# Optimization experiments

Hardware: AMD Instinct MI355X
Metric: run time of the kernel (lower is better)

## Reference

```python
import jax, jax.numpy as jnp
import numpy as np

T, B, I, H = 2048, 256, 64, 128


def setup_inputs() -> dict:
    key = jax.random.key(0)
    ks = jax.random.split(key, 12)
    s_i = 1.0 / np.sqrt(I)
    s_h = 1.0 / np.sqrt(H)
    return {
        "x": jax.random.normal(ks[0], (T, B, I), dtype=jnp.float32),
        # input->hidden kernels (with bias), flax GRUCell naming ir/iz/in
        "Wir": jax.random.normal(ks[1], (I, H), dtype=jnp.float32) * s_i,
        "Wiz": jax.random.normal(ks[2], (I, H), dtype=jnp.float32) * s_i,
        "Win": jax.random.normal(ks[3], (I, H), dtype=jnp.float32) * s_i,
        "bir": jnp.zeros((H,), dtype=jnp.float32),
        "biz": jnp.zeros((H,), dtype=jnp.float32),
        "bin": jnp.zeros((H,), dtype=jnp.float32),
        # hidden->hidden kernels: hr/hz no bias, hn has bias (flax GRUCell)
        "Whr": jax.random.normal(ks[4], (H, H), dtype=jnp.float32) * s_h,
        "Whz": jax.random.normal(ks[5], (H, H), dtype=jnp.float32) * s_h,
        "Whn": jax.random.normal(ks[6], (H, H), dtype=jnp.float32) * s_h,
        "bhn": jnp.zeros((H,), dtype=jnp.float32),
        # classifier Linear(H, 1)
        "Wc": jax.random.normal(ks[7], (H, 1), dtype=jnp.float32) * s_h,
        "bc": jnp.zeros((1,), dtype=jnp.float32),
    }


def reference(x, Wir, Wiz, Win, bir, biz, bin, Whr, Whz, Whn, bhn, Wc, bc):
    # GRU scan over time (time-major), flax GRUCell math:
    # r = sig(x Wir + bir + h Whr); z = sig(x Wiz + biz + h Whz)
    def step(h, xt):
        r = jax.nn.sigmoid(xt @ Wir + bir + h @ Whr)
        z = jax.nn.sigmoid(xt @ Wiz + biz + h @ Whz)
        n = jnp.tanh(xt @ Win + bin + r * (h @ Whn + bhn))
        h_new = (1.0 - z) * n + z * h
        return h_new, h_new

    h0 = jnp.zeros((x.shape[1], Whr.shape[0]), dtype=x.dtype)
    _, hs = jax.lax.scan(step, h0, x)  # hs: [T, B, H]
    return jax.nn.sigmoid(hs @ Wc + bc)  # [T, B, 1]
```

## Files before the change

kernel.cpp:

```cpp
#include <hip/hip_runtime.h>

#define TT 2048
#define BB 256
#define II 64
#define HH 128
#define CHP 16
#define NCH (TT / CHP)
#define GXS 532

#define LOG2E  1.4426950408889634f
#define LOG2E2 2.8853900817779268f

typedef __fp16 f16;
typedef __fp16 h2  __attribute__((ext_vector_type(2)));
typedef __fp16 v8h __attribute__((ext_vector_type(8)));
typedef float  v4f __attribute__((ext_vector_type(4)));
typedef int    v4i __attribute__((ext_vector_type(4)));

union HI { int i; h2 h; };
__device__ __forceinline__ h2  i2h(int v) { HI u; u.i = v; return u.h; }
__device__ __forceinline__ int h2i(h2 v)  { HI u; u.h = v; return u.i; }

__device__ __forceinline__ float fexp2(float x) {
  float r; asm("v_exp_f32 %0, %1" : "=v"(r) : "v"(x)); return r;
}
__device__ __forceinline__ float fsig(float x) {
  return __builtin_amdgcn_rcpf(1.0f + __expf(-x));
}

__device__ __forceinline__ void bar_lgkm() {
  asm volatile("s_waitcnt lgkmcnt(0)\n\ts_barrier" ::: "memory");
}

template <int CLS>
__global__ __launch_bounds__(512, 1) void gru_mfma(
    const float* __restrict__ x,
    const float* __restrict__ Wir, const float* __restrict__ Wiz, const float* __restrict__ Win,
    const float* __restrict__ bir, const float* __restrict__ biz, const float* __restrict__ bin_,
    const float* __restrict__ Whr, const float* __restrict__ Whz, const float* __restrict__ Whn,
    const float* __restrict__ bhn, const float* __restrict__ Wc,  const float* __restrict__ bc,
    f16* __restrict__ hh, float* __restrict__ out)
{
  const int t = threadIdx.x, b = blockIdx.x;
  const int w = t >> 6;
  const int l = t & 63;
  const int q = l >> 4;
  const int r = l & 15;
  const int nc = 16 * w + r;

  __shared__ __attribute__((aligned(16))) signed char hq8[2][HH];
  __shared__ __attribute__((aligned(16))) f16   xch[2][CHP][72];
  __shared__ __attribute__((aligned(16))) float gxb[2][CHP][GXS];
  __shared__ float cpart[2][128];

  v4i bqr[2], bqz[2], bqn[2];
  float invR, invZ, invN;
  {
    float mr = 1e-20f, mz = 1e-20f, mn = 1e-20f;
    for (int f = 0; f < 2; ++f)
      for (int j = 0; j < 16; ++j) {
        const int k = 64 * f + 16 * q + j;
        mr = fmaxf(mr, fabsf(Whr[k * HH + nc]));
        mz = fmaxf(mz, fabsf(Whz[k * HH + nc]));
        mn = fmaxf(mn, fabsf(Whn[k * HH + nc]));
      }
    mr = fmaxf(mr, __shfl_xor(mr, 16, 64)); mr = fmaxf(mr, __shfl_xor(mr, 32, 64));
    mz = fmaxf(mz, __shfl_xor(mz, 16, 64)); mz = fmaxf(mz, __shfl_xor(mz, 32, 64));
    mn = fmaxf(mn, __shfl_xor(mn, 16, 64)); mn = fmaxf(mn, __shfl_xor(mn, 32, 64));
    const float sr = 127.f / mr, sz = 127.f / mz, sn = 127.f / mn;
    invR = LOG2E  * mr / 16129.f;
    invZ = LOG2E  * mz / 16129.f;
    invN = LOG2E2 * mn / 16129.f;
    for (int f = 0; f < 2; ++f) {
      union { signed char c[16]; v4i v; } ur, uz, un;
      for (int j = 0; j < 16; ++j) {
        const int k = 64 * f + 16 * q + j;
        ur.c[j] = (signed char)(int)rintf(Whr[k * HH + nc] * sr);
        uz.c[j] = (signed char)(int)rintf(Whz[k * HH + nc] * sz);
        un.c[j] = (signed char)(int)rintf(Whn[k * HH + nc] * sn);
      }
      bqr[f] = ur.v; bqz[f] = uz.v; bqn[f] = un.v;
    }
  }

  v8h wir[2], wiz[2], win2[2];
  for (int kt = 0; kt < 2; ++kt) {
    v8h vr, vz, vn;
    for (int j = 0; j < 8; ++j) {
      const int kg = 32 * kt + 8 * q + j;
      vr[j] = (f16)(LOG2E  * Wir[kg * HH + nc]);
      vz[j] = (f16)(LOG2E  * Wiz[kg * HH + nc]);
      vn[j] = (f16)(LOG2E2 * Win[kg * HH + nc]);
    }
    wir[kt] = vr; wiz[kt] = vz; win2[kt] = vn;
  }

  const float birc = LOG2E * bir[nc],  bizc = LOG2E * biz[nc];
  const float binc = LOG2E2 * bin_[nc], bhnc = LOG2E2 * bhn[nc];
  float wc = 0.f, bc0 = 0.f;
  if (CLS == 1) { wc = Wc[nc]; bc0 = bc[0]; }

  auto precomp_full = [&](int pn, v8h ax0, v8h ax1) {
    v4f cr = {birc, birc, birc, birc};
    v4f cz = {bizc, bizc, bizc, bizc};
    v4f cn = {binc, binc, binc, binc};
    cr = __builtin_amdgcn_mfma_f32_16x16x32_f16(ax0, wir[0],  cr, 0, 0, 0);
    cz = __builtin_amdgcn_mfma_f32_16x16x32_f16(ax0, wiz[0],  cz, 0, 0, 0);
    cn = __builtin_amdgcn_mfma_f32_16x16x32_f16(ax0, win2[0], cn, 0, 0, 0);
    cr = __builtin_amdgcn_mfma_f32_16x16x32_f16(ax1, wir[1],  cr, 0, 0, 0);
    cz = __builtin_amdgcn_mfma_f32_16x16x32_f16(ax1, wiz[1],  cz, 0, 0, 0);
    cn = __builtin_amdgcn_mfma_f32_16x16x32_f16(ax1, win2[1], cn, 0, 0, 0);
    #pragma unroll
    for (int j = 0; j < 4; ++j) {
      v4f pk; pk[0] = cr[j]; pk[1] = cz[j]; pk[2] = cn[j]; pk[3] = 0.f;
      *(v4f*)&gxb[pn][4 * q + j][nc * 4] = pk;
    }
  };

  const int xrow = t >> 5, xcol = (t & 31) * 2;
  float2 xr;
  {
    float2 xA = *(const float2*)(x + ((size_t)(0   + xrow) * BB + b) * II + xcol);
    float2 xB = *(const float2*)(x + ((size_t)(CHP + xrow) * BB + b) * II + xcol);
    if (t < HH) { hq8[0][t] = 0; hq8[1][t] = 0; }
    *(int*)&xch[0][xrow][xcol] = h2i(__builtin_amdgcn_cvt_pkrtz(xA.x, xA.y));
    __syncthreads();
    {
      v8h a0x = *(const v8h*)&xch[0][r][8 * q];
      v8h a1x = *(const v8h*)&xch[0][r][32 + 8 * q];
      precomp_full(0, a0x, a1x);
    }
    *(int*)&xch[1][xrow][xcol] = h2i(__builtin_amdgcn_cvt_pkrtz(xB.x, xB.y));
    __syncthreads();
  }

  v4f gp = *(const v4f*)&gxb[0][0][nc * 4];

  v4i ai0 = {0, 0, 0, 0}, ai1 = {0, 0, 0, 0};
  float hst = 0.f;
  f16* hup = (CLS == 0) ? (hh + (size_t)b * HH) : nullptr;
  v4f cpr, cpz, cpn;

  for (int c = 0; c < NCH; ++c) {
    const int p = c & 1;
    const bool pc = (c + 1 < NCH);
    const bool ld = (c + 2 < NCH);

    v8h ax0 = {}, ax1 = {};
    if (pc) {
      ax0 = *(const v8h*)&xch[p ^ 1][r][8 * q];
      ax1 = *(const v8h*)&xch[p ^ 1][r][32 + 8 * q];
    }
    if (ld) {
      xr = *(const float2*)(x + ((size_t)((c + 2) * CHP + xrow) * BB + b) * II + xcol);
    }

    #pragma unroll
    for (int sc = 0; sc < CHP; ++sc) {
      const int s = c * CHP + sc;
      const int cur = sc & 1, nxt = cur ^ 1;

      if (r == 0) {
        ai0 = *(const v4i*)&hq8[cur][16 * q];
        ai1 = *(const v4i*)&hq8[cur][64 + 16 * q];
      }

      if (pc) {
        if (sc == 0) {
          v4f ir = {birc, birc, birc, birc};
          cpr = __builtin_amdgcn_mfma_f32_16x16x32_f16(ax0, wir[0], ir, 0, 0, 0);
        } else if (sc == 1) {
          v4f iz = {bizc, bizc, bizc, bizc};
          cpz = __builtin_amdgcn_mfma_f32_16x16x32_f16(ax0, wiz[0], iz, 0, 0, 0);
        } else if (sc == 2) {
          v4f in_ = {binc, binc, binc, binc};
          cpn = __builtin_amdgcn_mfma_f32_16x16x32_f16(ax0, win2[0], in_, 0, 0, 0);
        } else if (sc == 3) {
          cpr = __builtin_amdgcn_mfma_f32_16x16x32_f16(ax1, wir[1], cpr, 0, 0, 0);
        } else if (sc == 4) {
          cpz = __builtin_amdgcn_mfma_f32_16x16x32_f16(ax1, wiz[1], cpz, 0, 0, 0);
        } else if (sc == 5) {
          cpn = __builtin_amdgcn_mfma_f32_16x16x32_f16(ax1, win2[1], cpn, 0, 0, 0);
        } else if (sc >= 6 && sc < 10) {
          const int j = sc - 6;
          v4f pk; pk[0] = cpr[j]; pk[1] = cpz[j]; pk[2] = cpn[j]; pk[3] = 0.f;
          *(v4f*)&gxb[p ^ 1][4 * q + j][nc * 4] = pk;
        }
      }

      float cred = 0.f;
      if (CLS == 1 && w == 7 && (sc > 0 || c > 0))
        cred = cpart[nxt][l] + cpart[nxt][64 + l];

      const v4i zi = {0, 0, 0, 0};
      v4i cr_, cn2, cz_;
      cr_ = __builtin_amdgcn_mfma_i32_16x16x64_i8(ai0, bqr[0], zi, 0, 0, 0);
      cn2 = __builtin_amdgcn_mfma_i32_16x16x64_i8(ai0, bqn[0], zi, 0, 0, 0);
      cz_ = __builtin_amdgcn_mfma_i32_16x16x64_i8(ai0, bqz[0], zi, 0, 0, 0);
      cr_ = __builtin_amdgcn_mfma_i32_16x16x64_i8(ai1, bqr[1], cr_, 0, 0, 0);
      cn2 = __builtin_amdgcn_mfma_i32_16x16x64_i8(ai1, bqn[1], cn2, 0, 0, 0);
      cz_ = __builtin_amdgcn_mfma_i32_16x16x64_i8(ai1, bqz[1], cz_, 0, 0, 0);

      const v4f g = gp;
      if (sc < CHP - 1) {
        gp = *(const v4f*)&gxb[p][sc + 1][nc * 4];
      } else if (c + 1 < NCH) {
        gp = *(const v4f*)&gxb[p ^ 1][0][nc * 4];
      }

      if (q == 0) {
        const float arS = (float)cr_[0] * invR + g[0];
        const float rr  = __builtin_amdgcn_rcpf(1.f + fexp2(-arS));
        const float anS = (float)cn2[0] * invN + bhnc;
        const float nn  = 1.f - 2.f * __builtin_amdgcn_rcpf(1.f + fexp2(g[2] + rr * anS));
        const float azS = (float)cz_[0] * invZ + g[1];
        const float zz  = __builtin_amdgcn_rcpf(1.f + fexp2(-azS));
        hst = nn + zz * (hst - nn);
        hq8[nxt][nc] = (signed char)(int)rintf(hst * 127.f);
        if (CLS == 0) hup[nc] = (f16)hst;
        if (CLS == 1) cpart[cur][nc] = hst * wc;
      }
      if (CLS == 0) hup += BB * HH;

      if (CLS == 1 && w == 7 && (sc > 0 || c > 0)) {
        cred += __shfl_xor(cred, 1, 64);
        cred += __shfl_xor(cred, 2, 64);
        cred += __shfl_xor(cred, 4, 64);
        cred += __shfl_xor(cred, 8, 64);
        cred += __shfl_xor(cred, 16, 64);
        cred += __shfl_xor(cred, 32, 64);
        if (l == 0) out[(size_t)(s - 1) * BB + b] = fsig(cred + bc0);
      }

      if (sc == CHP - 1 && ld) {
        *(int*)&xch[p][xrow][xcol] = h2i(__builtin_amdgcn_cvt_pkrtz(xr.x, xr.y));
      }

      bar_lgkm();
    }
  }

  if (CLS == 1 && w == 7) {
    float cred = cpart[1][l] + cpart[1][64 + l];
    cred += __shfl_xor(cred, 1, 64);
    cred += __shfl_xor(cred, 2, 64);
    cred += __shfl_xor(cred, 4, 64);
    cred += __shfl_xor(cred, 8, 64);
    cred += __shfl_xor(cred, 16, 64);
    cred += __shfl_xor(cred, 32, 64);
    if (l == 0) out[(size_t)(TT - 1) * BB + b] = fsig(cred + bc0);
  }
}

__global__ __launch_bounds__(256) void gru_cls(
    const f16* __restrict__ hh, const float* __restrict__ Wc,
    const float* __restrict__ bc, float* __restrict__ out)
{
  const int t  = threadIdx.x;
  const int g4 = t & 3;
  const size_t row = (size_t)blockIdx.x * 64 + (t >> 2);
  const f16* hp = hh + row * HH + 32 * g4;
  const float* wp = Wc + 32 * g4;
  float acc = 0.f;
  #pragma unroll
  for (int i = 0; i < 4; ++i) {
    v8h h8 = *(const v8h*)(hp + 8 * i);
    const float* wq = wp + 8 * i;
    #pragma unroll
    for (int j = 0; j < 8; ++j) acc += (float)h8[j] * wq[j];
  }
  acc += __shfl_xor(acc, 1, 64);
  acc += __shfl_xor(acc, 2, 64);
  if (g4 == 0) out[row] = fsig(acc + bc[0]);
}

extern "C" void kernel_launch(void* const* d_in, const int* in_sizes, int n_in,
                              void* d_out, int out_size, void* d_ws, size_t ws_size,
                              hipStream_t stream) {
  const float* x    = (const float*)d_in[0];
  const float* Wir  = (const float*)d_in[1];
  const float* Wiz  = (const float*)d_in[2];
  const float* Win  = (const float*)d_in[3];
  const float* bir  = (const float*)d_in[4];
  const float* biz  = (const float*)d_in[5];
  const float* bin_ = (const float*)d_in[6];
  const float* Whr  = (const float*)d_in[7];
  const float* Whz  = (const float*)d_in[8];
  const float* Whn  = (const float*)d_in[9];
  const float* bhn  = (const float*)d_in[10];
  const float* Wc   = (const float*)d_in[11];
  const float* bc   = (const float*)d_in[12];
  float* out = (float*)d_out;

  const size_t need = (size_t)TT * BB * HH * sizeof(f16);
  if (d_ws != nullptr && ws_size >= need) {
    f16* hh = (f16*)d_ws;
    gru_mfma<0><<<dim3(BB), dim3(512), 0, stream>>>(
        x, Wir, Wiz, Win, bir, biz, bin_, Whr, Whz, Whn, bhn, Wc, bc, hh, out);
    gru_cls<<<dim3((TT * BB) / 64), dim3(256), 0, stream>>>(hh, Wc, bc, out);
  } else {
    gru_mfma<1><<<dim3(BB), dim3(512), 0, stream>>>(
        x, Wir, Wiz, Win, bir, biz, bin_, Whr, Whz, Whn, bhn, Wc, bc, nullptr, out);
  }
}
```

Before: 768.5 us.

## Fuse classifier into recurrent kernel, drop hidden-state workspace and second launch

Always uses the in-kernel classifier path: each step writes h*Wc partials to shared memory, and wave 7 reduces them one step later and writes the sigmoid output. This removes the f16 hidden-state writes to global memory and the separate classifier kernel launch. It also folds the sign negation into the r/z weights and biases so the per-step gate math saves a negate, and moves the cpart read earlier in the step. The cost is extra shared-memory traffic and shuffle reductions on wave 7 in every step of the serial loop.

New measurement: 1.126 ms. 1.46x slower.

```diff
diff --git a/kernel.cpp b/kernel.cpp
--- a/kernel.cpp
+++ b/kernel.cpp
@@ -24,22 +24,18 @@
 __device__ __forceinline__ float fexp2(float x) {
   float r; asm("v_exp_f32 %0, %1" : "=v"(r) : "v"(x)); return r;
 }
-__device__ __forceinline__ float fsig(float x) {
-  return __builtin_amdgcn_rcpf(1.0f + __expf(-x));
-}
 
 __device__ __forceinline__ void bar_lgkm() {
   asm volatile("s_waitcnt lgkmcnt(0)\n\ts_barrier" ::: "memory");
 }
 
-template <int CLS>
 __global__ __launch_bounds__(512, 1) void gru_mfma(
     const float* __restrict__ x,
     const float* __restrict__ Wir, const float* __restrict__ Wiz, const float* __restrict__ Win,
     const float* __restrict__ bir, const float* __restrict__ biz, const float* __restrict__ bin_,
     const float* __restrict__ Whr, const float* __restrict__ Whz, const float* __restrict__ Whn,
     const float* __restrict__ bhn, const float* __restrict__ Wc,  const float* __restrict__ bc,
-    f16* __restrict__ hh, float* __restrict__ out)
+    float* __restrict__ out)
 {
   const int t = threadIdx.x, b = blockIdx.x;
   const int w = t >> 6;
@@ -54,7 +50,7 @@
   __shared__ float cpart[2][128];
 
   v4i bqr[2], bqz[2], bqn[2];
-  float invR, invZ, invN;
+  float nivR, nivZ, invN;
   {
     float mr = 1e-20f, mz = 1e-20f, mn = 1e-20f;
     for (int f = 0; f < 2; ++f)
@@ -68,9 +64,9 @@
     mz = fmaxf(mz, __shfl_xor(mz, 16, 64)); mz = fmaxf(mz, __shfl_xor(mz, 32, 64));
     mn = fmaxf(mn, __shfl_xor(mn, 16, 64)); mn = fmaxf(mn, __shfl_xor(mn, 32, 64));
     const float sr = 127.f / mr, sz = 127.f / mz, sn = 127.f / mn;
-    invR = LOG2E  * mr / 16129.f;
-    invZ = LOG2E  * mz / 16129.f;
-    invN = LOG2E2 * mn / 16129.f;
+    nivR = -LOG2E * mr / 16129.f;
+    nivZ = -LOG2E * mz / 16129.f;
+    invN =  LOG2E2 * mn / 16129.f;
     for (int f = 0; f < 2; ++f) {
       union { signed char c[16]; v4i v; } ur, uz, un;
       for (int j = 0; j < 16; ++j) {
@@ -88,17 +84,17 @@
     v8h vr, vz, vn;
     for (int j = 0; j < 8; ++j) {
       const int kg = 32 * kt + 8 * q + j;
-      vr[j] = (f16)(LOG2E  * Wir[kg * HH + nc]);
-      vz[j] = (f16)(LOG2E  * Wiz[kg * HH + nc]);
-      vn[j] = (f16)(LOG2E2 * Win[kg * HH + nc]);
+      vr[j] = (f16)(-LOG2E  * Wir[kg * HH + nc]);
+      vz[j] = (f16)(-LOG2E  * Wiz[kg * HH + nc]);
+      vn[j] = (f16)( LOG2E2 * Win[kg * HH + nc]);
     }
     wir[kt] = vr; wiz[kt] = vz; win2[kt] = vn;
   }
 
-  const float birc = LOG2E * bir[nc],  bizc = LOG2E * biz[nc];
+  const float birc = -LOG2E * bir[nc],  bizc = -LOG2E * biz[nc];
   const float binc = LOG2E2 * bin_[nc], bhnc = LOG2E2 * bhn[nc];
-  float wc = 0.f, bc0 = 0.f;
-  if (CLS == 1) { wc = Wc[nc]; bc0 = bc[0]; }
+  const float wcp = Wc[nc];
+  const float bcp = LOG2E * bc[0];
 
   auto precomp_full = [&](int pn, v8h ax0, v8h ax1) {
     v4f cr = {birc, birc, birc, birc};
@@ -138,7 +134,6 @@
 
   v4i ai0 = {0, 0, 0, 0}, ai1 = {0, 0, 0, 0};
   float hst = 0.f;
-  f16* hup = (CLS == 0) ? (hh + (size_t)b * HH) : nullptr;
   v4f cpr, cpz, cpn;
 
   for (int c = 0; c < NCH; ++c) {
@@ -164,6 +159,10 @@
         ai0 = *(const v4i*)&hq8[cur][16 * q];
         ai1 = *(const v4i*)&hq8[cur][64 + 16 * q];
       }
+
+      float cred = 0.f;
+      if (w == 7 && (sc > 0 || c > 0))
+        cred = cpart[nxt][l] + cpart[nxt][64 + l];
 
       if (pc) {
         if (sc == 0) {
@@ -188,10 +187,6 @@
         }
       }
 
-      float cred = 0.f;
-      if (CLS == 1 && w == 7 && (sc > 0 || c > 0))
-        cred = cpart[nxt][l] + cpart[nxt][64 + l];
-
       const v4i zi = {0, 0, 0, 0};
       v4i cr_, cn2, cz_;
       cr_ = __builtin_amdgcn_mfma_i32_16x16x64_i8(ai0, bqr[0], zi, 0, 0, 0);
@@ -209,27 +204,25 @@
       }
 
       if (q == 0) {
-        const float arS = (float)cr_[0] * invR + g[0];
-        const float rr  = __builtin_amdgcn_rcpf(1.f + fexp2(-arS));
+        const float rr  = __builtin_amdgcn_rcpf(1.f + fexp2((float)cr_[0] * nivR + g[0]));
         const float anS = (float)cn2[0] * invN + bhnc;
         const float nn  = 1.f - 2.f * __builtin_amdgcn_rcpf(1.f + fexp2(g[2] + rr * anS));
-        const float azS = (float)cz_[0] * invZ + g[1];
-        const float zz  = __builtin_amdgcn_rcpf(1.f + fexp2(-azS));
+        const float zz  = __builtin_amdgcn_rcpf(1.f + fexp2((float)cz_[0] * nivZ + g[1]));
         hst = nn + zz * (hst - nn);
         hq8[nxt][nc] = (signed char)(int)rintf(hst * 127.f);
-        if (CLS == 0) hup[nc] = (f16)hst;
-        if (CLS == 1) cpart[cur][nc] = hst * wc;
-      }
-      if (CLS == 0) hup += BB * HH;
-
-      if (CLS == 1 && w == 7 && (sc > 0 || c > 0)) {
+        cpart[cur][nc] = hst * wcp;
+      }
+
+      if (w == 7 && (sc > 0 || c > 0)) {
         cred += __shfl_xor(cred, 1, 64);
         cred += __shfl_xor(cred, 2, 64);
         cred += __shfl_xor(cred, 4, 64);
         cred += __shfl_xor(cred, 8, 64);
         cred += __shfl_xor(cred, 16, 64);
         cred += __shfl_xor(cred, 32, 64);
-        if (l == 0) out[(size_t)(s - 1) * BB + b] = fsig(cred + bc0);
+        if (l == 0)
+          out[(size_t)(s - 1) * BB + b] =
+              __builtin_amdgcn_rcpf(1.f + fexp2(-(LOG2E * cred + bcp)));
       }
 
       if (sc == CHP - 1 && ld) {
@@ -240,7 +233,7 @@
     }
   }
 
-  if (CLS == 1 && w == 7) {
+  if (w == 7) {
     float cred = cpart[1][l] + cpart[1][64 + l];
     cred += __shfl_xor(cred, 1, 64);
     cred += __shfl_xor(cred, 2, 64);
@@ -248,30 +241,10 @@
     cred += __shfl_xor(cred, 8, 64);
     cred += __shfl_xor(cred, 16, 64);
     cred += __shfl_xor(cred, 32, 64);
-    if (l == 0) out[(size_t)(TT - 1) * BB + b] = fsig(cred + bc0);
-  }
-}
-
-__global__ __launch_bounds__(256) void gru_cls(
-    const f16* __restrict__ hh, const float* __restrict__ Wc,
-    const float* __restrict__ bc, float* __restrict__ out)
-{
-  const int t  = threadIdx.x;
-  const int g4 = t & 3;
-  const size_t row = (size_t)blockIdx.x * 64 + (t >> 2);
-  const f16* hp = hh + row * HH + 32 * g4;
-  const float* wp = Wc + 32 * g4;
-  float acc = 0.f;
-  #pragma unroll
-  for (int i = 0; i < 4; ++i) {
-    v8h h8 = *(const v8h*)(hp + 8 * i);
-    const float* wq = wp + 8 * i;
-    #pragma unroll
-    for (int j = 0; j < 8; ++j) acc += (float)h8[j] * wq[j];
-  }
-  acc += __shfl_xor(acc, 1, 64);
-  acc += __shfl_xor(acc, 2, 64);
-  if (g4 == 0) out[row] = fsig(acc + bc[0]);
+    if (l == 0)
+      out[(size_t)(TT - 1) * BB + b] =
+          __builtin_amdgcn_rcpf(1.f + fexp2(-(LOG2E * cred + bcp)));
+  }
 }
 
 extern "C" void kernel_launch(void* const* d_in, const int* in_sizes, int n_in,
@@ -292,14 +265,6 @@
   const float* bc   = (const float*)d_in[12];
   float* out = (float*)d_out;
 
-  const size_t need = (size_t)TT * BB * HH * sizeof(f16);
-  if (d_ws != nullptr && ws_size >= need) {
-    f16* hh = (f16*)d_ws;
-    gru_mfma<0><<<dim3(BB), dim3(512), 0, stream>>>(
-        x, Wir, Wiz, Win, bir, biz, bin_, Whr, Whz, Whn, bhn, Wc, bc, hh, out);
-    gru_cls<<<dim3((TT * BB) / 64), dim3(256), 0, stream>>>(hh, Wc, bc, out);
-  } else {
-    gru_mfma<1><<<dim3(BB), dim3(512), 0, stream>>>(
-        x, Wir, Wiz, Win, bir, biz, bin_, Whr, Whz, Whn, bhn, Wc, bc, nullptr, out);
-  }
-}
+  gru_mfma<<<dim3(BB), dim3(512), 0, stream>>>(
+      x, Wir, Wiz, Win, bir, biz, bin_, Whr, Whz, Whn, bhn, Wc, bc, out);
+}
```

## Specialize warps: four compute recurrence, four handle input projection and classifier

Applied to the files above, without the earlier changes.

The 8 waves are split into two roles. Waves 0-3 each run the int8 hidden-state MFMAs and gate math for 32 hidden units (two 16-column tiles). Waves 4-7 do the input-projection MFMAs, the x staging (now float4 loads), and the classifier reduction, which now reads the int8 hidden state directly instead of a separate cpart buffer. The aim is to take the side work off the critical recurrence path. In exchange, each compute wave does twice the MFMA and transcendental work per step, and the classifier output now uses quantized h.

After: 885.4 us. +15.2%, slower.

```diff
diff --git a/kernel.cpp b/kernel.cpp
--- a/kernel.cpp
+++ b/kernel.cpp
@@ -46,113 +46,134 @@
   const int l = t & 63;
   const int q = l >> 4;
   const int r = l & 15;
-  const int nc = 16 * w + r;
+  const bool isC = (w < 4);
+  const int hw = w & 3;
 
   __shared__ __attribute__((aligned(16))) signed char hq8[2][HH];
   __shared__ __attribute__((aligned(16))) f16   xch[2][CHP][72];
   __shared__ __attribute__((aligned(16))) float gxb[2][CHP][GXS];
-  __shared__ float cpart[2][128];
-
-  v4i bqr[2], bqz[2], bqn[2];
-  float invR, invZ, invN;
+
+  v4i bqr[2][2], bqz[2][2], bqn[2][2];
+  float invR[2], invZ[2], invN[2], bhnc[2];
+  v8h hwr[2][2], hwz[2][2], hwn[2][2];
+  float birc[2], bizc[2], binc[2];
+  float wcA = 0.f, wcB = 0.f, bc0 = 0.f;
+
+  if (isC) {
+    for (int ct = 0; ct < 2; ++ct) {
+      const int n = 32 * w + 16 * ct + r;
+      float mr = 1e-20f, mz = 1e-20f, mn = 1e-20f;
+      for (int f = 0; f < 2; ++f)
+        for (int j = 0; j < 16; ++j) {
+          const int k = 64 * f + 16 * q + j;
+          mr = fmaxf(mr, fabsf(Whr[k * HH + n]));
+          mz = fmaxf(mz, fabsf(Whz[k * HH + n]));
+          mn = fmaxf(mn, fabsf(Whn[k * HH + n]));
+        }
+      mr = fmaxf(mr, __shfl_xor(mr, 16, 64)); mr = fmaxf(mr, __shfl_xor(mr, 32, 64));
+      mz = fmaxf(mz, __shfl_xor(mz, 16, 64)); mz = fmaxf(mz, __shfl_xor(mz, 32, 64));
+      mn = fmaxf(mn, __shfl_xor(mn, 16, 64)); mn = fmaxf(mn, __shfl_xor(mn, 32, 64));
+      const float sr = 127.f / mr, sz = 127.f / mz, sn = 127.f / mn;
+      invR[ct] = LOG2E  * mr / 16129.f;
+      invZ[ct] = LOG2E  * mz / 16129.f;
+      invN[ct] = LOG2E2 * mn / 16129.f;
+      bhnc[ct] = LOG2E2 * bhn[n];
+      for (int f = 0; f < 2; ++f) {
+        union { signed char c[16]; v4i v; } ur, uz, un;
+        for (int j = 0; j < 16; ++j) {
+          const int k = 64 * f + 16 * q + j;
+          ur.c[j] = (signed char)(int)rintf(Whr[k * HH + n] * sr);
+          uz.c[j] = (signed char)(int)rintf(Whz[k * HH + n] * sz);
+          un.c[j] = (signed char)(int)rintf(Whn[k * HH + n] * sn);
+        }
+        bqr[ct][f] = ur.v; bqz[ct][f] = uz.v; bqn[ct][f] = un.v;
+      }
+    }
+  } else {
+    for (int ct = 0; ct < 2; ++ct) {
+      const int n = 32 * hw + 16 * ct + r;
+      for (int kt = 0; kt < 2; ++kt) {
+        v8h vr, vz, vn;
+        for (int j = 0; j < 8; ++j) {
+          const int kg = 32 * kt + 8 * q + j;
+          vr[j] = (f16)(LOG2E  * Wir[kg * HH + n]);
+          vz[j] = (f16)(LOG2E  * Wiz[kg * HH + n]);
+          vn[j] = (f16)(LOG2E2 * Win[kg * HH + n]);
+        }
+        hwr[ct][kt] = vr; hwz[ct][kt] = vz; hwn[ct][kt] = vn;
+      }
+      birc[ct] = LOG2E * bir[n]; bizc[ct] = LOG2E * biz[n]; binc[ct] = LOG2E2 * bin_[n];
+    }
+    if (CLS == 1 && w == 4) {
+      wcA = Wc[2 * l] / 127.f; wcB = Wc[2 * l + 1] / 127.f; bc0 = bc[0];
+    }
+  }
+
+  auto precomp_full = [&](int pn, v8h ax0, v8h ax1) {
+    #pragma unroll
+    for (int ct = 0; ct < 2; ++ct) {
+      const int n = 32 * hw + 16 * ct + r;
+      v4f cr = {birc[ct], birc[ct], birc[ct], birc[ct]};
+      v4f cz = {bizc[ct], bizc[ct], bizc[ct], bizc[ct]};
+      v4f cn = {binc[ct], binc[ct], binc[ct], binc[ct]};
+      cr = __builtin_amdgcn_mfma_f32_16x16x32_f16(ax0, hwr[ct][0], cr, 0, 0, 0);
+      cz = __builtin_amdgcn_mfma_f32_16x16x32_f16(ax0, hwz[ct][0], cz, 0, 0, 0);
+      cn = __builtin_amdgcn_mfma_f32_16x16x32_f16(ax0, hwn[ct][0], cn, 0, 0, 0);
+      cr = __builtin_amdgcn_mfma_f32_16x16x32_f16(ax1, hwr[ct][1], cr, 0, 0, 0);
+      cz = __builtin_amdgcn_mfma_f32_16x16x32_f16(ax1, hwz[ct][1], cz, 0, 0, 0);
+      cn = __builtin_amdgcn_mfma_f32_16x16x32_f16(ax1, hwn[ct][1], cn, 0, 0, 0);
+      #pragma unroll
+      for (int j = 0; j < 4; ++j) {
+        v4f pk; pk[0] = cr[j]; pk[1] = cz[j]; pk[2] = cn[j]; pk[3] = 0.f;
+        *(v4f*)&gxb[pn][4 * q + j][n * 4] = pk;
+      }
+    }
+  };
+
   {
-    float mr = 1e-20f, mz = 1e-20f, mn = 1e-20f;
-    for (int f = 0; f < 2; ++f)
-      for (int j = 0; j < 16; ++j) {
-        const int k = 64 * f + 16 * q + j;
-        mr = fmaxf(mr, fabsf(Whr[k * HH + nc]));
-        mz = fmaxf(mz, fabsf(Whz[k * HH + nc]));
-        mn = fmaxf(mn, fabsf(Whn[k * HH + nc]));
-      }
-    mr = fmaxf(mr, __shfl_xor(mr, 16, 64)); mr = fmaxf(mr, __shfl_xor(mr, 32, 64));
-    mz = fmaxf(mz, __shfl_xor(mz, 16, 64)); mz = fmaxf(mz, __shfl_xor(mz, 32, 64));
-    mn = fmaxf(mn, __shfl_xor(mn, 16, 64)); mn = fmaxf(mn, __shfl_xor(mn, 32, 64));
-    const float sr = 127.f / mr, sz = 127.f / mz, sn = 127.f / mn;
-    invR = LOG2E  * mr / 16129.f;
-    invZ = LOG2E  * mz / 16129.f;
-    invN = LOG2E2 * mn / 16129.f;
-    for (int f = 0; f < 2; ++f) {
-      union { signed char c[16]; v4i v; } ur, uz, un;
-      for (int j = 0; j < 16; ++j) {
-        const int k = 64 * f + 16 * q + j;
-        ur.c[j] = (signed char)(int)rintf(Whr[k * HH + nc] * sr);
-        uz.c[j] = (signed char)(int)rintf(Whz[k * HH + nc] * sz);
-        un.c[j] = (signed char)(int)rintf(Whn[k * HH + nc] * sn);
-      }
-      bqr[f] = ur.v; bqz[f] = uz.v; bqn[f] = un.v;
-    }
-  }
-
-  v8h wir[2], wiz[2], win2[2];
-  for (int kt = 0; kt < 2; ++kt) {
-    v8h vr, vz, vn;
-    for (int j = 0; j < 8; ++j) {
-      const int kg = 32 * kt + 8 * q + j;
-      vr[j] = (f16)(LOG2E  * Wir[kg * HH + nc]);
-      vz[j] = (f16)(LOG2E  * Wiz[kg * HH + nc]);
-      vn[j] = (f16)(LOG2E2 * Win[kg * HH + nc]);
-    }
-    wir[kt] = vr; wiz[kt] = vz; win2[kt] = vn;
-  }
-
-  const float birc = LOG2E * bir[nc],  bizc = LOG2E * biz[nc];
-  const float binc = LOG2E2 * bin_[nc], bhnc = LOG2E2 * bhn[nc];
-  float wc = 0.f, bc0 = 0.f;
-  if (CLS == 1) { wc = Wc[nc]; bc0 = bc[0]; }
-
-  auto precomp_full = [&](int pn, v8h ax0, v8h ax1) {
-    v4f cr = {birc, birc, birc, birc};
-    v4f cz = {bizc, bizc, bizc, bizc};
-    v4f cn = {binc, binc, binc, binc};
-    cr = __builtin_amdgcn_mfma_f32_16x16x32_f16(ax0, wir[0],  cr, 0, 0, 0);
-    cz = __builtin_amdgcn_mfma_f32_16x16x32_f16(ax0, wiz[0],  cz, 0, 0, 0);
-    cn = __builtin_amdgcn_mfma_f32_16x16x32_f16(ax0, win2[0], cn, 0, 0, 0);
-    cr = __builtin_amdgcn_mfma_f32_16x16x32_f16(ax1, wir[1],  cr, 0, 0, 0);
-    cz = __builtin_amdgcn_mfma_f32_16x16x32_f16(ax1, wiz[1],  cz, 0, 0, 0);
-    cn = __builtin_amdgcn_mfma_f32_16x16x32_f16(ax1, win2[1], cn, 0, 0, 0);
-    #pragma unroll
-    for (int j = 0; j < 4; ++j) {
-      v4f pk; pk[0] = cr[j]; pk[1] = cz[j]; pk[2] = cn[j]; pk[3] = 0.f;
-      *(v4f*)&gxb[pn][4 * q + j][nc * 4] = pk;
-    }
-  };
-
-  const int xrow = t >> 5, xcol = (t & 31) * 2;
-  float2 xr;
-  {
-    float2 xA = *(const float2*)(x + ((size_t)(0   + xrow) * BB + b) * II + xcol);
-    float2 xB = *(const float2*)(x + ((size_t)(CHP + xrow) * BB + b) * II + xcol);
+    const int pxr = t >> 5, pxc = (t & 31) * 2;
+    float2 xA = *(const float2*)(x + ((size_t)(0   + pxr) * BB + b) * II + pxc);
+    float2 xB = *(const float2*)(x + ((size_t)(CHP + pxr) * BB + b) * II + pxc);
     if (t < HH) { hq8[0][t] = 0; hq8[1][t] = 0; }
-    *(int*)&xch[0][xrow][xcol] = h2i(__builtin_amdgcn_cvt_pkrtz(xA.x, xA.y));
+    *(int*)&xch[0][pxr][pxc] = h2i(__builtin_amdgcn_cvt_pkrtz(xA.x, xA.y));
     __syncthreads();
-    {
+    if (!isC) {
       v8h a0x = *(const v8h*)&xch[0][r][8 * q];
       v8h a1x = *(const v8h*)&xch[0][r][32 + 8 * q];
       precomp_full(0, a0x, a1x);
     }
-    *(int*)&xch[1][xrow][xcol] = h2i(__builtin_amdgcn_cvt_pkrtz(xB.x, xB.y));
+    *(int*)&xch[1][pxr][pxc] = h2i(__builtin_amdgcn_cvt_pkrtz(xB.x, xB.y));
     __syncthreads();
   }
 
-  v4f gp = *(const v4f*)&gxb[0][0][nc * 4];
+  v4f gp0 = {0.f, 0.f, 0.f, 0.f}, gp1 = {0.f, 0.f, 0.f, 0.f};
+  if (isC) {
+    gp0 = *(const v4f*)&gxb[0][0][(32 * w + r) * 4];
+    gp1 = *(const v4f*)&gxb[0][0][(32 * w + 16 + r) * 4];
+  }
 
   v4i ai0 = {0, 0, 0, 0}, ai1 = {0, 0, 0, 0};
-  float hst = 0.f;
+  float hst[2] = {0.f, 0.f};
   f16* hup = (CLS == 0) ? (hh + (size_t)b * HH) : nullptr;
   v4f cpr, cpz, cpn;
+  v8h ax0 = {}, ax1 = {};
+  float4 xr;
+  const int hxr = (t >> 4) & 15, hxc = (t & 15) * 4;
+  const v4i zi = {0, 0, 0, 0};
 
   for (int c = 0; c < NCH; ++c) {
     const int p = c & 1;
     const bool pc = (c + 1 < NCH);
     const bool ld = (c + 2 < NCH);
 
-    v8h ax0 = {}, ax1 = {};
-    if (pc) {
-      ax0 = *(const v8h*)&xch[p ^ 1][r][8 * q];
-      ax1 = *(const v8h*)&xch[p ^ 1][r][32 + 8 * q];
-    }
-    if (ld) {
-      xr = *(const float2*)(x + ((size_t)((c + 2) * CHP + xrow) * BB + b) * II + xcol);
+    if (!isC) {
+      if (pc) {
+        ax0 = *(const v8h*)&xch[p ^ 1][r][8 * q];
+        ax1 = *(const v8h*)&xch[p ^ 1][r][32 + 8 * q];
+      }
+      if (ld) {
+        xr = *(const float4*)(x + ((size_t)((c + 2) * CHP + hxr) * BB + b) * II + hxc);
+      }
     }
 
     #pragma unroll
@@ -160,88 +181,128 @@
       const int s = c * CHP + sc;
       const int cur = sc & 1, nxt = cur ^ 1;
 
-      if (r == 0) {
-        ai0 = *(const v4i*)&hq8[cur][16 * q];
-        ai1 = *(const v4i*)&hq8[cur][64 + 16 * q];
-      }
-
-      if (pc) {
-        if (sc == 0) {
-          v4f ir = {birc, birc, birc, birc};
-          cpr = __builtin_amdgcn_mfma_f32_16x16x32_f16(ax0, wir[0], ir, 0, 0, 0);
-        } else if (sc == 1) {
-          v4f iz = {bizc, bizc, bizc, bizc};
-          cpz = __builtin_amdgcn_mfma_f32_16x16x32_f16(ax0, wiz[0], iz, 0, 0, 0);
-        } else if (sc == 2) {
-          v4f in_ = {binc, binc, binc, binc};
-          cpn = __builtin_amdgcn_mfma_f32_16x16x32_f16(ax0, win2[0], in_, 0, 0, 0);
-        } else if (sc == 3) {
-          cpr = __builtin_amdgcn_mfma_f32_16x16x32_f16(ax1, wir[1], cpr, 0, 0, 0);
-        } else if (sc == 4) {
-          cpz = __builtin_amdgcn_mfma_f32_16x16x32_f16(ax1, wiz[1], cpz, 0, 0, 0);
-        } else if (sc == 5) {
-          cpn = __builtin_amdgcn_mfma_f32_16x16x32_f16(ax1, win2[1], cpn, 0, 0, 0);
-        } else if (sc >= 6 && sc < 10) {
-          const int j = sc - 6;
-          v4f pk; pk[0] = cpr[j]; pk[1] = cpz[j]; pk[2] = cpn[j]; pk[3] = 0.f;
-          *(v4f*)&gxb[p ^ 1][4 * q + j][nc * 4] = pk;
-        }
-      }
-
-      float cred = 0.f;
-      if (CLS == 1 && w == 7 && (sc > 0 || c > 0))
-        cred = cpart[nxt][l] + cpart[nxt][64 + l];
-
-      const v4i zi = {0, 0, 0, 0};
-      v4i cr_, cn2, cz_;
-      cr_ = __builtin_amdgcn_mfma_i32_16x16x64_i8(ai0, bqr[0], zi, 0, 0, 0);
-      cn2 = __builtin_amdgcn_mfma_i32_16x16x64_i8(ai0, bqn[0], zi, 0, 0, 0);
-      cz_ = __builtin_amdgcn_mfma_i32_16x16x64_i8(ai0, bqz[0], zi, 0, 0, 0);
-      cr_ = __builtin_amdgcn_mfma_i32_16x16x64_i8(ai1, bqr[1], cr_, 0, 0, 0);
-      cn2 = __builtin_amdgcn_mfma_i32_16x16x64_i8(ai1, bqn[1], cn2, 0, 0, 0);
-      cz_ = __builtin_amdgcn_mfma_i32_16x16x64_i8(ai1, bqz[1], cz_, 0, 0, 0);
-
-      const v4f g = gp;
-      if (sc < CHP - 1) {
-        gp = *(const v4f*)&gxb[p][sc + 1][nc * 4];
-      } else if (c + 1 < NCH) {
-        gp = *(const v4f*)&gxb[p ^ 1][0][nc * 4];
-      }
-
-      if (q == 0) {
-        const float arS = (float)cr_[0] * invR + g[0];
-        const float rr  = __builtin_amdgcn_rcpf(1.f + fexp2(-arS));
-        const float anS = (float)cn2[0] * invN + bhnc;
-        const float nn  = 1.f - 2.f * __builtin_amdgcn_rcpf(1.f + fexp2(g[2] + rr * anS));
-        const float azS = (float)cz_[0] * invZ + g[1];
-        const float zz  = __builtin_amdgcn_rcpf(1.f + fexp2(-azS));
-        hst = nn + zz * (hst - nn);
-        hq8[nxt][nc] = (signed char)(int)rintf(hst * 127.f);
-        if (CLS == 0) hup[nc] = (f16)hst;
-        if (CLS == 1) cpart[cur][nc] = hst * wc;
-      }
-      if (CLS == 0) hup += BB * HH;
-
-      if (CLS == 1 && w == 7 && (sc > 0 || c > 0)) {
-        cred += __shfl_xor(cred, 1, 64);
-        cred += __shfl_xor(cred, 2, 64);
-        cred += __shfl_xor(cred, 4, 64);
-        cred += __shfl_xor(cred, 8, 64);
-        cred += __shfl_xor(cred, 16, 64);
-        cred += __shfl_xor(cred, 32, 64);
-        if (l == 0) out[(size_t)(s - 1) * BB + b] = fsig(cred + bc0);
-      }
-
-      if (sc == CHP - 1 && ld) {
-        *(int*)&xch[p][xrow][xcol] = h2i(__builtin_amdgcn_cvt_pkrtz(xr.x, xr.y));
+      if (isC) {
+        if (r == 0) {
+          ai0 = *(const v4i*)&hq8[cur][16 * q];
+          ai1 = *(const v4i*)&hq8[cur][64 + 16 * q];
+        }
+
+        v4i cr0, cr1, cn0, cn1, cz0, cz1;
+        cr0 = __builtin_amdgcn_mfma_i32_16x16x64_i8(ai0, bqr[0][0], zi, 0, 0, 0);
+        cr1 = __builtin_amdgcn_mfma_i32_16x16x64_i8(ai0, bqr[1][0], zi, 0, 0, 0);
+        cn0 = __builtin_amdgcn_mfma_i32_16x16x64_i8(ai0, bqn[0][0], zi, 0, 0, 0);
+        cn1 = __builtin_amdgcn_mfma_i32_16x16x64_i8(ai0, bqn[1][0], zi, 0, 0, 0);
+        cz0 = __builtin_amdgcn_mfma_i32_16x16x64_i8(ai0, bqz[0][0], zi, 0, 0, 0);
+        cz1 = __builtin_amdgcn_mfma_i32_16x16x64_i8(ai0, bqz[1][0], zi, 0, 0, 0);
+        cr0 = __builtin_amdgcn_mfma_i32_16x16x64_i8(ai1, bqr[0][1], cr0, 0, 0, 0);
+        cr1 = __builtin_amdgcn_mfma_i32_16x16x64_i8(ai1, bqr[1][1], cr1, 0, 0, 0);
+        cn0 = __builtin_amdgcn_mfma_i32_16x16x64_i8(ai1, bqn[0][1], cn0, 0, 0, 0);
+        cn1 = __builtin_amdgcn_mfma_i32_16x16x64_i8(ai1, bqn[1][1], cn1, 0, 0, 0);
+        cz0 = __builtin_amdgcn_mfma_i32_16x16x64_i8(ai1, bqz[0][1], cz0, 0, 0, 0);
+        cz1 = __builtin_amdgcn_mfma_i32_16x16x64_i8(ai1, bqz[1][1], cz1, 0, 0, 0);
+
+        const v4f g0 = gp0, g1 = gp1;
+        if (sc < CHP - 1) {
+          gp0 = *(const v4f*)&gxb[p][sc + 1][(32 * w + r) * 4];
+          gp1 = *(const v4f*)&gxb[p][sc + 1][(32 * w + 16 + r) * 4];
+        } else if (c + 1 < NCH) {
+          gp0 = *(const v4f*)&gxb[p ^ 1][0][(32 * w + r) * 4];
+          gp1 = *(const v4f*)&gxb[p ^ 1][0][(32 * w + 16 + r) * 4];
+        }
+
+        if (q == 0) {
+          {
+            const float arS = (float)cr0[0] * invR[0] + g0[0];
+            const float rr  = __builtin_amdgcn_rcpf(1.f + fexp2(-arS));
+            const float anS = (float)cn0[0] * invN[0] + bhnc[0];
+            const float nn  = 1.f - 2.f * __builtin_amdgcn_rcpf(1.f + fexp2(g0[2] + rr * anS));
+            const float azS = (float)cz0[0] * invZ[0] + g0[1];
+            const float zz  = __builtin_amdgcn_rcpf(1.f + fexp2(-azS));
+            hst[0] = nn + zz * (hst[0] - nn);
+            hq8[nxt][32 * w + r] = (signed char)(int)rintf(hst[0] * 127.f);
+            if (CLS == 0) hup[32 * w + r] = (f16)hst[0];
+          }
+          {
+            const float arS = (float)cr1[0] * invR[1] + g1[0];
+            const float rr  = __builtin_amdgcn_rcpf(1.f + fexp2(-arS));
+            const float anS = (float)cn1[0] * invN[1] + bhnc[1];
+            const float nn  = 1.f - 2.f * __builtin_amdgcn_rcpf(1.f + fexp2(g1[2] + rr * anS));
+            const float azS = (float)cz1[0] * invZ[1] + g1[1];
+            const float zz  = __builtin_amdgcn_rcpf(1.f + fexp2(-azS));
+            hst[1] = nn + zz * (hst[1] - nn);
+            hq8[nxt][32 * w + 16 + r] = (signed char)(int)rintf(hst[1] * 127.f);
+            if (CLS == 0) hup[32 * w + 16 + r] = (f16)hst[1];
+          }
+        }
+        if (CLS == 0) hup += BB * HH;
+      } else {
+        if (pc) {
+          if (sc == 0) {
+            v4f i0 = {birc[0], birc[0], birc[0], birc[0]};
+            v4f i1 = {bizc[0], bizc[0], bizc[0], bizc[0]};
+            cpr = __builtin_amdgcn_mfma_f32_16x16x32_f16(ax0, hwr[0][0], i0, 0, 0, 0);
+            cpz = __builtin_amdgcn_mfma_f32_16x16x32_f16(ax0, hwz[0][0], i1, 0, 0, 0);
+          } else if (sc == 1) {
+            v4f i2 = {binc[0], binc[0], binc[0], binc[0]};
+            cpn = __builtin_amdgcn_mfma_f32_16x16x32_f16(ax0, hwn[0][0], i2, 0, 0, 0);
+            cpr = __builtin_amdgcn_mfma_f32_16x16x32_f16(ax1, hwr[0][1], cpr, 0, 0, 0);
+          } else if (sc == 2) {
+            cpz = __builtin_amdgcn_mfma_f32_16x16x32_f16(ax1, hwz[0][1], cpz, 0, 0, 0);
+            cpn = __builtin_amdgcn_mfma_f32_16x16x32_f16(ax1, hwn[0][1], cpn, 0, 0, 0);
+          } else if (sc == 3) {
+            const int n = 32 * hw + r;
+            #pragma unroll
+            for (int j = 0; j < 4; ++j) {
+              v4f pk; pk[0] = cpr[j]; pk[1] = cpz[j]; pk[2] = cpn[j]; pk[3] = 0.f;
+              *(v4f*)&gxb[p ^ 1][4 * q + j][n * 4] = pk;
+            }
+          } else if (sc == 4) {
+            v4f i0 = {birc[1], birc[1], birc[1], birc[1]};
+            v4f i1 = {bizc[1], bizc[1], bizc[1], bizc[1]};
+            cpr = __builtin_amdgcn_mfma_f32_16x16x32_f16(ax0, hwr[1][0], i0, 0, 0, 0);
+            cpz = __builtin_amdgcn_mfma_f32_16x16x32_f16(ax0, hwz[1][0], i1, 0, 0, 0);
+          } else if (sc == 5) {
+            v4f i2 = {binc[1], binc[1], binc[1], binc[1]};
+            cpn = __builtin_amdgcn_mfma_f32_16x16x32_f16(ax0, hwn[1][0], i2, 0, 0, 0);
+            cpr = __builtin_amdgcn_mfma_f32_16x16x32_f16(ax1, hwr[1][1], cpr, 0, 0, 0);
+          } else if (sc == 6) {
+            cpz = __builtin_amdgcn_mfma_f32_16x16x32_f16(ax1, hwz[1][1], cpz, 0, 0, 0);
+            cpn = __builtin_amdgcn_mfma_f32_16x16x32_f16(ax1, hwn[1][1], cpn, 0, 0, 0);
+          } else if (sc == 7) {
+            const int n = 32 * hw + 16 + r;
+            #pragma unroll
+            for (int j = 0; j < 4; ++j) {
+              v4f pk; pk[0] = cpr[j]; pk[1] = cpz[j]; pk[2] = cpn[j]; pk[3] = 0.f;
+              *(v4f*)&gxb[p ^ 1][4 * q + j][n * 4] = pk;
+            }
+          }
+        }
+        if (sc == CHP - 1 && ld) {
+          int2 pv;
+          pv.x = h2i(__builtin_amdgcn_cvt_pkrtz(xr.x, xr.y));
+          pv.y = h2i(__builtin_amdgcn_cvt_pkrtz(xr.z, xr.w));
+          *(int2*)&xch[p][hxr][hxc] = pv;
+        }
+        if (CLS == 1 && w == 4 && (sc > 0 || c > 0)) {
+          const int hv = *(const short*)&hq8[cur][2 * l];
+          float cred = (float)((hv << 24) >> 24) * wcA + (float)(hv >> 8) * wcB;
+          cred += __shfl_xor(cred, 1, 64);
+          cred += __shfl_xor(cred, 2, 64);
+          cred += __shfl_xor(cred, 4, 64);
+          cred += __shfl_xor(cred, 8, 64);
+          cred += __shfl_xor(cred, 16, 64);
+          cred += __shfl_xor(cred, 32, 64);
+          if (l == 0) out[(size_t)(s - 1) * BB + b] = fsig(cred + bc0);
+        }
       }
 
       bar_lgkm();
     }
   }
 
-  if (CLS == 1 && w == 7) {
-    float cred = cpart[1][l] + cpart[1][64 + l];
+  if (CLS == 1 && w == 4) {
+    const int hv = *(const short*)&hq8[0][2 * l];
+    float cred = (float)((hv << 24) >> 24) * wcA + (float)(hv >> 8) * wcB;
     cred += __shfl_xor(cred, 1, 64);
     cred += __shfl_xor(cred, 2, 64);
     cred += __shfl_xor(cred, 4, 64);
```
